# Performance work log

Hardware: AMD Instinct MI355X
Metric: run time of the kernel (lower is better)

The kernel has to match this reference:

```python
import jax, jax.numpy as jnp
import numpy as np

N_NODES, N_EDGES, D_FEAT, HIDDEN, N_CLASSES = 100000, 3200000, 128, 16, 40


def setup_inputs() -> dict:
    key = jax.random.key(0)
    ks = jax.random.split(key, 6)
    x = jax.random.normal(ks[0], (N_NODES, D_FEAT), dtype=jnp.float32)
    edge_index = jax.random.randint(ks[1], (2, N_EDGES), 0, N_NODES, dtype=jnp.int32)
    # SAGEConv params: lin_l (aggregated neighbors, with bias), lin_r (root, no bias)
    W_l = jax.random.normal(ks[2], (D_FEAT, HIDDEN), dtype=jnp.float32) / np.sqrt(D_FEAT)
    b_l = jnp.zeros((HIDDEN,), jnp.float32)
    W_r = jax.random.normal(ks[3], (D_FEAT, HIDDEN), dtype=jnp.float32) / np.sqrt(D_FEAT)
    # final Linear(hidden, num_classes)
    W3 = jax.random.normal(ks[4], (HIDDEN, N_CLASSES), dtype=jnp.float32) / np.sqrt(HIDDEN)
    b3 = jnp.zeros((N_CLASSES,), jnp.float32)
    return {"x": x, "edge_index": edge_index, "W_l": W_l, "b_l": b_l,
            "W_r": W_r, "W3": W3, "b3": b3}


def reference(x, edge_index, W_l, b_l, W_r, W3, b3):
    N = x.shape[0]
    src, dst = edge_index[0], edge_index[1]
    # mean aggregation of source features onto target nodes (PyG source_to_target)
    agg = jax.ops.segment_sum(x[src], dst, num_segments=N)            # [N, F]
    deg = jax.ops.segment_sum(jnp.ones_like(dst, dtype=x.dtype), dst, num_segments=N)
    mean = agg / jnp.maximum(deg, 1.0)[:, None]                        # zero-in-degree -> 0
    # SAGEConv: lin_l(mean) + lin_r(x)
    h = mean @ W_l + b_l + x @ W_r                                     # [N, 16]
    h = jax.nn.relu(h)
    logits = h @ W3 + b3                                               # [N, C]
    return jax.nn.log_softmax(logits, axis=1)
```

## Files before the change

### kernel.cpp

```cpp
#include <hip/hip_runtime.h>
#include <hip/hip_bf16.h>

#define D_FEAT 128
#define HIDDEN 16
#define NCLS 40
#define EPB 4096
#define QSCALE 32.0f
#define QBIAS  8.0f

typedef unsigned int uint;

__global__ __launch_bounds__(256) void p1lin_kernel(
    const int* __restrict__ src, const int* __restrict__ dst,
    int* __restrict__ gcur1, int* __restrict__ buf1,
    int E, int C, int R1, int nb1,
    const float* __restrict__ x,
    const float* __restrict__ Wl, const float* __restrict__ Wr,
    uint* __restrict__ ylb, float* __restrict__ yr, int N) {
  __shared__ __align__(16) char smem[33280];
  int tid = threadIdx.x;

  if (blockIdx.x < nb1) {
    int* lh    = (int*)smem;
    int* loff  = lh + 32;
    int* gbase = loff + 32;
    int* lbuf  = gbase + 32;
    int* ldst  = lbuf + 4096;
    if (tid < 32) lh[tid] = 0;
    __syncthreads();

    int base = blockIdx.x * EPB;
    int key[16], rnk[16], rec[16];
#pragma unroll
    for (int j = 0; j < 16; ++j) {
      int e = base + j * 256 + tid;
      bool ok = e < E;
      int d = ok ? dst[e] : 0;
      int s = ok ? src[e] : 0;
      key[j] = ok ? (d >> 12) : -1;
      rec[j] = s | ((d & 4095) << 17);
      if (ok) rnk[j] = atomicAdd(&lh[key[j]], 1);
    }
    __syncthreads();

    if (tid < 64) {
      int v = (tid < 32) ? lh[tid] : 0;
      int inc = v;
#pragma unroll
      for (int dd = 1; dd < 32; dd <<= 1) {
        int t = __shfl_up(inc, dd);
        if ((int)tid >= dd) inc += t;
      }
      if (tid < 32) {
        loff[tid] = inc - v;
        gbase[tid] = (v && tid < C) ? atomicAdd(&gcur1[tid], v) : 0;
      }
    }
    __syncthreads();

#pragma unroll
    for (int j = 0; j < 16; ++j) {
      if (key[j] >= 0) {
        int p = loff[key[j]] + rnk[j];
        lbuf[p] = rec[j];
        int gp = gbase[key[j]] + rnk[j];
        ldst[p] = (gp < R1) ? key[j] * R1 + gp : -1;
      }
    }
    __syncthreads();

    int tot = min(EPB, E - base);
    for (int i = tid; i < tot; i += 256) {
      int di = ldst[i];
      if (di >= 0) buf1[di] = lbuf[i];
    }
  } else {
    float (*sW)[8][4] = (float(*)[8][4])smem;
    float (*sx)[132]  = (float(*)[132])(smem + 16384);

    for (int idx = tid; idx < D_FEAT * 32; idx += 256) {
      int k = idx >> 5, o = idx & 31;
      float v = (o < 16) ? Wl[k * 16 + o] : Wr[k * 16 + (o - 16)];
      sW[k][o >> 2][o & 3] = v;
    }

    int row0 = (blockIdx.x - nb1) * 32;
    for (int q = tid; q < 32 * 32; q += 256) {
      int r = q >> 5, k4 = q & 31;
      int row = row0 + r;
      float4 v = make_float4(0.f, 0.f, 0.f, 0.f);
      if (row < N) v = *(const float4*)(x + (size_t)row * D_FEAT + k4 * 4);
      *(float4*)(&sx[r][k4 * 4]) = v;
    }
    __syncthreads();

    int r = tid >> 3, oq = tid & 7;
    int row = row0 + r;
    if (row < N) {
      float4 acc = make_float4(0.f, 0.f, 0.f, 0.f);
#pragma unroll
      for (int k = 0; k < D_FEAT; ++k) {
        float xv = sx[r][k];
        const float4 w = *(const float4*)(&sW[k][oq][0]);
        acc.x += xv * w.x; acc.y += xv * w.y;
        acc.z += xv * w.z; acc.w += xv * w.w;
      }
      if (oq < 4) {
        int q0 = __float2int_rn((fminf(fmaxf(acc.x, -7.9f), 7.9f) + QBIAS) * QSCALE);
        int q1 = __float2int_rn((fminf(fmaxf(acc.y, -7.9f), 7.9f) + QBIAS) * QSCALE);
        int q2 = __float2int_rn((fminf(fmaxf(acc.z, -7.9f), 7.9f) + QBIAS) * QSCALE);
        int q3 = __float2int_rn((fminf(fmaxf(acc.w, -7.9f), 7.9f) + QBIAS) * QSCALE);
        uint2 pk;
        pk.x = (uint)q0 | ((uint)q1 << 16);
        pk.y = (uint)q2 | ((uint)q3 << 16);
        *(uint2*)(ylb + (size_t)row * 8 + oq * 2) = pk;
      } else {
        *(float4*)(yr + (size_t)row * 16 + (oq - 4) * 4) = acc;
      }
    }
  }
}

__global__ __launch_bounds__(256) void pass2_kernel(
    const int* __restrict__ buf1, const int* __restrict__ gcur1,
    int* __restrict__ gcur, int* __restrict__ packed,
    int C, int R1, int RF, int chunks) {
  int c = blockIdx.x / chunks;
  int chunk = blockIdx.x - c * chunks;
  int cnt1 = min(gcur1[c], R1);
  int base = chunk * EPB;
  int tot = cnt1 - base;
  if (tot <= 0) return;
  tot = min(tot, EPB);

  __shared__ int lh[32], loff[32], gbase[32];
  __shared__ int lbuf[EPB];
  __shared__ int ldst[EPB];
  int tid = threadIdx.x;
  if (tid < 32) lh[tid] = 0;
  __syncthreads();

  const int* in = buf1 + (size_t)c * R1 + base;
  int key[16], rnk[16], rec[16];
#pragma unroll
  for (int j = 0; j < 16; ++j) {
    int i = j * 256 + tid;
    bool ok = i < tot;
    int r = ok ? in[i] : 0;
    int d12 = (r >> 17) & 4095;
    key[j] = ok ? (d12 >> 7) : -1;
    rec[j] = (r & 0x1FFFF) | ((d12 & 127) << 20);
    if (ok) rnk[j] = atomicAdd(&lh[key[j]], 1);
  }
  __syncthreads();

  if (tid < 64) {
    int v = (tid < 32) ? lh[tid] : 0;
    int inc = v;
#pragma unroll
    for (int dd = 1; dd < 32; dd <<= 1) {
      int t = __shfl_up(inc, dd);
      if ((int)tid >= dd) inc += t;
    }
    if (tid < 32) {
      loff[tid] = inc - v;
      gbase[tid] = v ? atomicAdd(&gcur[c * 32 + tid], v) : 0;
    }
  }
  __syncthreads();

#pragma unroll
  for (int j = 0; j < 16; ++j) {
    if (key[j] >= 0) {
      int p = loff[key[j]] + rnk[j];
      lbuf[p] = rec[j];
      int gp = gbase[key[j]] + rnk[j];
      ldst[p] = (gp < RF) ? (c * 32 + key[j]) * RF + gp : -1;
    }
  }
  __syncthreads();

  for (int i = tid; i < tot; i += 256) {
    int di = ldst[i];
    if (di >= 0) packed[di] = lbuf[i];
  }
}

__global__ __launch_bounds__(1024) void baggrf_kernel(
    const uint* __restrict__ ylb, const int* __restrict__ packed,
    const int* __restrict__ gcur, const float* __restrict__ yr,
    const float* __restrict__ bl, const float* __restrict__ W3,
    const float* __restrict__ b3, float* __restrict__ out,
    int N, int RF) {
  __shared__ uint sagg[128 * 9];
  __shared__ int sdeg[128];
  __shared__ float syr[128 * 16];
  __shared__ float sW3[16 * NCLS];
  __shared__ float sb3[NCLS];
  __shared__ float sbl[16];
  int tid = threadIdx.x;
  int b = blockIdx.x;
  int node0 = b * 128;

  for (int i = tid; i < 128 * 9; i += 1024) sagg[i] = 0u;
  if (tid < 128) sdeg[tid] = 0;
  if (tid >= 384 && tid < 1024) sW3[tid - 384] = W3[tid - 384];
  if (tid < NCLS) sb3[tid] = b3[tid];
  if (tid >= 64 && tid < 80) sbl[tid - 64] = bl[tid - 64];
  __syncthreads();

  int cnt = min(gcur[b], RF);
  int lo = b * RF, hi = lo + cnt;
  for (int e = lo + tid; e < hi; e += 2048) {
    int eb = e + 1024;
    bool has2 = eb < hi;
    int p0 = packed[e];
    int p1 = packed[has2 ? eb : e];
    int s0 = p0 & 0xFFFFF, d0 = (p0 >> 20) & 127;
    int s1 = p1 & 0xFFFFF, d1 = (p1 >> 20) & 127;
    const uint4* q0 = (const uint4*)(ylb + (size_t)s0 * 8);
    const uint4* q1 = (const uint4*)(ylb + (size_t)s1 * 8);
    uint4 a0 = q0[0], a1 = q0[1];
    uint4 b0 = q1[0], b1 = q1[1];

    uint* ip0 = &sagg[d0 * 9];
    atomicAdd(ip0 + 0, a0.x); atomicAdd(ip0 + 1, a0.y);
    atomicAdd(ip0 + 2, a0.z); atomicAdd(ip0 + 3, a0.w);
    atomicAdd(ip0 + 4, a1.x); atomicAdd(ip0 + 5, a1.y);
    atomicAdd(ip0 + 6, a1.z); atomicAdd(ip0 + 7, a1.w);
    atomicAdd(&sdeg[d0], 1);
    if (has2) {
      uint* ip1 = &sagg[d1 * 9];
      atomicAdd(ip1 + 0, b0.x); atomicAdd(ip1 + 1, b0.y);
      atomicAdd(ip1 + 2, b0.z); atomicAdd(ip1 + 3, b0.w);
      atomicAdd(ip1 + 4, b1.x); atomicAdd(ip1 + 5, b1.y);
      atomicAdd(ip1 + 6, b1.z); atomicAdd(ip1 + 7, b1.w);
      atomicAdd(&sdeg[d1], 1);
    }
  }

  int nvalid = min(128, N - node0);
  if (nvalid > 0) {
    int tot16 = nvalid * 16;
    for (int i = tid; i < tot16; i += 1024)
      syr[i] = yr[(size_t)node0 * 16 + i];
  }
  __syncthreads();

  int node = tid >> 3, q = tid & 7;
  int n = node0 + node;
  if (n < N) {
    int dg = sdeg[node];
    float bsub = (QBIAS * QSCALE) * (float)dg;
    float inv = 1.0f / (QSCALE * fmaxf((float)dg, 1.0f));
    float h[16];
#pragma unroll
    for (int j = 0; j < 8; ++j) {
      uint s = sagg[node * 9 + j];
      float v0 = ((float)(s & 0xFFFFu) - bsub) * inv;
      float v1 = ((float)(s >> 16) - bsub) * inv;
      h[2 * j]     = fmaxf(v0 + sbl[2 * j]     + syr[node * 16 + 2 * j], 0.f);
      h[2 * j + 1] = fmaxf(v1 + sbl[2 * j + 1] + syr[node * 16 + 2 * j + 1], 0.f);
    }
    float lg[5];
#pragma unroll
    for (int j = 0; j < 5; ++j) lg[j] = sb3[q * 5 + j];
#pragma unroll
    for (int k = 0; k < 16; ++k) {
      float hv = h[k];
#pragma unroll
      for (int j = 0; j < 5; ++j) lg[j] += hv * sW3[k * NCLS + q * 5 + j];
    }
    float m = lg[0];
#pragma unroll
    for (int j = 1; j < 5; ++j) m = fmaxf(m, lg[j]);
#pragma unroll
    for (int dd = 1; dd < 8; dd <<= 1) m = fmaxf(m, __shfl_xor(m, dd));
    float s = 0.f;
#pragma unroll
    for (int j = 0; j < 5; ++j) s += __expf(lg[j] - m);
#pragma unroll
    for (int dd = 1; dd < 8; dd <<= 1) s += __shfl_xor(s, dd);
    float lse = m + __logf(s);
    float* op = out + (size_t)n * NCLS + q * 5;
#pragma unroll
    for (int j = 0; j < 5; ++j) op[j] = lg[j] - lse;
  }
}

extern "C" void kernel_launch(void* const* d_in, const int* in_sizes, int n_in,
                              void* d_out, int out_size, void* d_ws, size_t ws_size,
                              hipStream_t stream) {
  const float* x   = (const float*)d_in[0];
  const int* eidx  = (const int*)d_in[1];
  const float* Wl  = (const float*)d_in[2];
  const float* bl  = (const float*)d_in[3];
  const float* Wr  = (const float*)d_in[4];
  const float* W3  = (const float*)d_in[5];
  const float* b3  = (const float*)d_in[6];
  float* out = (float*)d_out;

  int N = in_sizes[0] / D_FEAT;
  int E = in_sizes[1] / 2;
  const int* src = eidx;
  const int* dst = eidx + E;

  int C = (N + 4095) >> 12;
  int chunks = (E / C) / EPB + 2;
  int R1 = chunks * EPB;
  int Bf = C * 32;
  int B = (N + 127) >> 7;
  long long m = (long long)E * 128 / N;
  int RF = (int)((m + m / 8 + 511) / 512 * 512);

  size_t n16 = (size_t)N * 16;
  uint* ylb   = (uint*)d_ws;
  float* yr   = (float*)(ylb + (size_t)N * 8);
  int* gcur   = (int*)(yr + n16);
  int* gcur1  = gcur + Bf;
  int* buf1   = gcur1 + C;
  int* packed = buf1 + (size_t)C * R1;

  hipMemsetAsync(gcur, 0, (size_t)(Bf + C) * sizeof(int), stream);

  int nb1 = (E + EPB - 1) / EPB;
  int nblin = (N + 31) / 32;
  p1lin_kernel<<<nb1 + nblin, 256, 0, stream>>>(src, dst, gcur1, buf1,
                                                E, C, R1, nb1,
                                                x, Wl, Wr, ylb, yr, N);

  pass2_kernel<<<C * chunks, 256, 0, stream>>>(buf1, gcur1, gcur, packed,
                                               C, R1, RF, chunks);

  baggrf_kernel<<<B, 1024, 0, stream>>>(ylb, packed, gcur, yr, bl, W3, b3,
                                        out, N, RF);
}
```

Baseline: 95.92 us.

## Move dense linear into pass2 kernel and register-tile rows per thread

Pass 1 now runs as a standalone edge-bucketing kernel, and the dense x@[Wl|Wr] projection is fused into the pass-2 launch instead of pass 1. This balances work between the two launches and shrinks pass-1 shared memory. The linear path now computes 4 rows per thread, reading x straight from global memory rather than staging it in LDS, and pass 2 derives scatter destinations on the fly instead of keeping an ldst array, which halves its LDS use. The trade-off is more registers per thread and uncached global reads of x.

New measurement: 97.83 us. Within noise of the previous version (+2.0%).

```diff
diff --git a/kernel.cpp b/kernel.cpp
--- a/kernel.cpp
+++ b/kernel.cpp
@@ -10,129 +10,14 @@
 
 typedef unsigned int uint;
 
-__global__ __launch_bounds__(256) void p1lin_kernel(
+__device__ __forceinline__ void fma4(float4& a, float s, const float4 w) {
+  a.x += s * w.x; a.y += s * w.y; a.z += s * w.z; a.w += s * w.w;
+}
+
+__global__ __launch_bounds__(256) void pass1_kernel(
     const int* __restrict__ src, const int* __restrict__ dst,
     int* __restrict__ gcur1, int* __restrict__ buf1,
-    int E, int C, int R1, int nb1,
-    const float* __restrict__ x,
-    const float* __restrict__ Wl, const float* __restrict__ Wr,
-    uint* __restrict__ ylb, float* __restrict__ yr, int N) {
-  __shared__ __align__(16) char smem[33280];
-  int tid = threadIdx.x;
-
-  if (blockIdx.x < nb1) {
-    int* lh    = (int*)smem;
-    int* loff  = lh + 32;
-    int* gbase = loff + 32;
-    int* lbuf  = gbase + 32;
-    int* ldst  = lbuf + 4096;
-    if (tid < 32) lh[tid] = 0;
-    __syncthreads();
-
-    int base = blockIdx.x * EPB;
-    int key[16], rnk[16], rec[16];
-#pragma unroll
-    for (int j = 0; j < 16; ++j) {
-      int e = base + j * 256 + tid;
-      bool ok = e < E;
-      int d = ok ? dst[e] : 0;
-      int s = ok ? src[e] : 0;
-      key[j] = ok ? (d >> 12) : -1;
-      rec[j] = s | ((d & 4095) << 17);
-      if (ok) rnk[j] = atomicAdd(&lh[key[j]], 1);
-    }
-    __syncthreads();
-
-    if (tid < 64) {
-      int v = (tid < 32) ? lh[tid] : 0;
-      int inc = v;
-#pragma unroll
-      for (int dd = 1; dd < 32; dd <<= 1) {
-        int t = __shfl_up(inc, dd);
-        if ((int)tid >= dd) inc += t;
-      }
-      if (tid < 32) {
-        loff[tid] = inc - v;
-        gbase[tid] = (v && tid < C) ? atomicAdd(&gcur1[tid], v) : 0;
-      }
-    }
-    __syncthreads();
-
-#pragma unroll
-    for (int j = 0; j < 16; ++j) {
-      if (key[j] >= 0) {
-        int p = loff[key[j]] + rnk[j];
-        lbuf[p] = rec[j];
-        int gp = gbase[key[j]] + rnk[j];
-        ldst[p] = (gp < R1) ? key[j] * R1 + gp : -1;
-      }
-    }
-    __syncthreads();
-
-    int tot = min(EPB, E - base);
-    for (int i = tid; i < tot; i += 256) {
-      int di = ldst[i];
-      if (di >= 0) buf1[di] = lbuf[i];
-    }
-  } else {
-    float (*sW)[8][4] = (float(*)[8][4])smem;
-    float (*sx)[132]  = (float(*)[132])(smem + 16384);
-
-    for (int idx = tid; idx < D_FEAT * 32; idx += 256) {
-      int k = idx >> 5, o = idx & 31;
-      float v = (o < 16) ? Wl[k * 16 + o] : Wr[k * 16 + (o - 16)];
-      sW[k][o >> 2][o & 3] = v;
-    }
-
-    int row0 = (blockIdx.x - nb1) * 32;
-    for (int q = tid; q < 32 * 32; q += 256) {
-      int r = q >> 5, k4 = q & 31;
-      int row = row0 + r;
-      float4 v = make_float4(0.f, 0.f, 0.f, 0.f);
-      if (row < N) v = *(const float4*)(x + (size_t)row * D_FEAT + k4 * 4);
-      *(float4*)(&sx[r][k4 * 4]) = v;
-    }
-    __syncthreads();
-
-    int r = tid >> 3, oq = tid & 7;
-    int row = row0 + r;
-    if (row < N) {
-      float4 acc = make_float4(0.f, 0.f, 0.f, 0.f);
-#pragma unroll
-      for (int k = 0; k < D_FEAT; ++k) {
-        float xv = sx[r][k];
-        const float4 w = *(const float4*)(&sW[k][oq][0]);
-        acc.x += xv * w.x; acc.y += xv * w.y;
-        acc.z += xv * w.z; acc.w += xv * w.w;
-      }
-      if (oq < 4) {
-        int q0 = __float2int_rn((fminf(fmaxf(acc.x, -7.9f), 7.9f) + QBIAS) * QSCALE);
-        int q1 = __float2int_rn((fminf(fmaxf(acc.y, -7.9f), 7.9f) + QBIAS) * QSCALE);
-        int q2 = __float2int_rn((fminf(fmaxf(acc.z, -7.9f), 7.9f) + QBIAS) * QSCALE);
-        int q3 = __float2int_rn((fminf(fmaxf(acc.w, -7.9f), 7.9f) + QBIAS) * QSCALE);
-        uint2 pk;
-        pk.x = (uint)q0 | ((uint)q1 << 16);
-        pk.y = (uint)q2 | ((uint)q3 << 16);
-        *(uint2*)(ylb + (size_t)row * 8 + oq * 2) = pk;
-      } else {
-        *(float4*)(yr + (size_t)row * 16 + (oq - 4) * 4) = acc;
-      }
-    }
-  }
-}
-
-__global__ __launch_bounds__(256) void pass2_kernel(
-    const int* __restrict__ buf1, const int* __restrict__ gcur1,
-    int* __restrict__ gcur, int* __restrict__ packed,
-    int C, int R1, int RF, int chunks) {
-  int c = blockIdx.x / chunks;
-  int chunk = blockIdx.x - c * chunks;
-  int cnt1 = min(gcur1[c], R1);
-  int base = chunk * EPB;
-  int tot = cnt1 - base;
-  if (tot <= 0) return;
-  tot = min(tot, EPB);
-
+    int E, int C, int R1) {
   __shared__ int lh[32], loff[32], gbase[32];
   __shared__ int lbuf[EPB];
   __shared__ int ldst[EPB];
@@ -140,16 +25,16 @@
   if (tid < 32) lh[tid] = 0;
   __syncthreads();
 
-  const int* in = buf1 + (size_t)c * R1 + base;
+  int base = blockIdx.x * EPB;
   int key[16], rnk[16], rec[16];
 #pragma unroll
   for (int j = 0; j < 16; ++j) {
-    int i = j * 256 + tid;
-    bool ok = i < tot;
-    int r = ok ? in[i] : 0;
-    int d12 = (r >> 17) & 4095;
-    key[j] = ok ? (d12 >> 7) : -1;
-    rec[j] = (r & 0x1FFFF) | ((d12 & 127) << 20);
+    int e = base + j * 256 + tid;
+    bool ok = e < E;
+    int d = ok ? dst[e] : 0;
+    int s = ok ? src[e] : 0;
+    key[j] = ok ? (d >> 12) : -1;
+    rec[j] = s | ((d & 4095) << 17);
     if (ok) rnk[j] = atomicAdd(&lh[key[j]], 1);
   }
   __syncthreads();
@@ -164,7 +49,7 @@
     }
     if (tid < 32) {
       loff[tid] = inc - v;
-      gbase[tid] = v ? atomicAdd(&gcur[c * 32 + tid], v) : 0;
+      gbase[tid] = (v && tid < C) ? atomicAdd(&gcur1[tid], v) : 0;
     }
   }
   __syncthreads();
@@ -175,14 +60,152 @@
       int p = loff[key[j]] + rnk[j];
       lbuf[p] = rec[j];
       int gp = gbase[key[j]] + rnk[j];
-      ldst[p] = (gp < RF) ? (c * 32 + key[j]) * RF + gp : -1;
-    }
-  }
-  __syncthreads();
-
+      ldst[p] = (gp < R1) ? key[j] * R1 + gp : -1;
+    }
+  }
+  __syncthreads();
+
+  int tot = min(EPB, E - base);
   for (int i = tid; i < tot; i += 256) {
     int di = ldst[i];
-    if (di >= 0) packed[di] = lbuf[i];
+    if (di >= 0) buf1[di] = lbuf[i];
+  }
+}
+
+__global__ __launch_bounds__(256) void p2lin_kernel(
+    const int* __restrict__ buf1, const int* __restrict__ gcur1,
+    int* __restrict__ gcur, int* __restrict__ packed,
+    int C, int R1, int RF, int chunks, int nb2,
+    const float* __restrict__ x,
+    const float* __restrict__ Wl, const float* __restrict__ Wr,
+    uint* __restrict__ ylb, float* __restrict__ yr, int N) {
+  __shared__ __align__(16) char smem[16896];
+  int tid = threadIdx.x;
+
+  if ((int)blockIdx.x < nb2) {
+    int* lbuf  = (int*)smem;
+    int* lh    = (int*)(smem + 16384);
+    int* loff  = lh + 32;
+    int* gbase = loff + 32;
+
+    int c = blockIdx.x / chunks;
+    int chunk = blockIdx.x - c * chunks;
+    int cnt1 = min(gcur1[c], R1);
+    int base = chunk * EPB;
+    int tot = cnt1 - base;
+    if (tot <= 0) return;
+    tot = min(tot, EPB);
+
+    if (tid < 32) lh[tid] = 0;
+    __syncthreads();
+
+    const int* in = buf1 + (size_t)c * R1 + base;
+    int key[16], rnk[16], rec[16];
+#pragma unroll
+    for (int j = 0; j < 16; ++j) {
+      int i = j * 256 + tid;
+      bool ok = i < tot;
+      int r = ok ? in[i] : 0;
+      key[j] = ok ? ((r >> 24) & 31) : -1;
+      rec[j] = r;
+      if (ok) rnk[j] = atomicAdd(&lh[key[j]], 1);
+    }
+    __syncthreads();
+
+    if (tid < 64) {
+      int v = (tid < 32) ? lh[tid] : 0;
+      int inc = v;
+#pragma unroll
+      for (int dd = 1; dd < 32; dd <<= 1) {
+        int t = __shfl_up(inc, dd);
+        if ((int)tid >= dd) inc += t;
+      }
+      if (tid < 32) {
+        loff[tid] = inc - v;
+        gbase[tid] = v ? atomicAdd(&gcur[c * 32 + tid], v) : 0;
+      }
+    }
+    __syncthreads();
+
+#pragma unroll
+    for (int j = 0; j < 16; ++j)
+      if (key[j] >= 0) lbuf[loff[key[j]] + rnk[j]] = rec[j];
+    __syncthreads();
+
+    for (int i = tid; i < tot; i += 256) {
+      int r = lbuf[i];
+      int k = (r >> 24) & 31;
+      int gp = gbase[k] + (i - loff[k]);
+      if (gp < RF) {
+        int d12 = (r >> 17) & 4095;
+        packed[(size_t)(c * 32 + k) * RF + gp] =
+            (r & 0x1FFFF) | ((d12 & 127) << 20);
+      }
+    }
+  } else {
+    float* sW = (float*)smem;
+    const float4* sWf4 = (const float4*)smem;
+
+    for (int i = tid; i < 4096; i += 256) {
+      int k = i >> 5, c = i & 31;
+      sW[i] = (c < 16) ? Wl[k * 16 + c] : Wr[k * 16 + (c - 16)];
+    }
+    __syncthreads();
+
+    int row0 = ((int)blockIdx.x - nb2) * 128;
+    int quad = tid & 7, rg = tid >> 3;
+    int r0 = row0 + rg * 4;
+    int rr0 = min(r0 + 0, N - 1), rr1 = min(r0 + 1, N - 1);
+    int rr2 = min(r0 + 2, N - 1), rr3 = min(r0 + 3, N - 1);
+    const float* xp0 = x + (size_t)rr0 * D_FEAT;
+    const float* xp1 = x + (size_t)rr1 * D_FEAT;
+    const float* xp2 = x + (size_t)rr2 * D_FEAT;
+    const float* xp3 = x + (size_t)rr3 * D_FEAT;
+
+    float4 acc0 = {0,0,0,0}, acc1 = {0,0,0,0}, acc2 = {0,0,0,0}, acc3 = {0,0,0,0};
+#pragma unroll 4
+    for (int k4 = 0; k4 < 32; ++k4) {
+      float4 x0 = *(const float4*)(xp0 + k4 * 4);
+      float4 x1 = *(const float4*)(xp1 + k4 * 4);
+      float4 x2 = *(const float4*)(xp2 + k4 * 4);
+      float4 x3 = *(const float4*)(xp3 + k4 * 4);
+      float4 w0 = sWf4[(k4 * 4 + 0) * 8 + quad];
+      fma4(acc0, x0.x, w0); fma4(acc1, x1.x, w0);
+      fma4(acc2, x2.x, w0); fma4(acc3, x3.x, w0);
+      float4 w1 = sWf4[(k4 * 4 + 1) * 8 + quad];
+      fma4(acc0, x0.y, w1); fma4(acc1, x1.y, w1);
+      fma4(acc2, x2.y, w1); fma4(acc3, x3.y, w1);
+      float4 w2 = sWf4[(k4 * 4 + 2) * 8 + quad];
+      fma4(acc0, x0.z, w2); fma4(acc1, x1.z, w2);
+      fma4(acc2, x2.z, w2); fma4(acc3, x3.z, w2);
+      float4 w3 = sWf4[(k4 * 4 + 3) * 8 + quad];
+      fma4(acc0, x0.w, w3); fma4(acc1, x1.w, w3);
+      fma4(acc2, x2.w, w3); fma4(acc3, x3.w, w3);
+    }
+
+    float4 accs[4] = {acc0, acc1, acc2, acc3};
+    if (quad < 4) {
+#pragma unroll
+      for (int r = 0; r < 4; ++r) {
+        if (r0 + r < N) {
+          float4 a = accs[r];
+          int q0 = __float2int_rn((fminf(fmaxf(a.x, -7.9f), 7.9f) + QBIAS) * QSCALE);
+          int q1 = __float2int_rn((fminf(fmaxf(a.y, -7.9f), 7.9f) + QBIAS) * QSCALE);
+          int q2 = __float2int_rn((fminf(fmaxf(a.z, -7.9f), 7.9f) + QBIAS) * QSCALE);
+          int q3 = __float2int_rn((fminf(fmaxf(a.w, -7.9f), 7.9f) + QBIAS) * QSCALE);
+          uint2 pk;
+          pk.x = (uint)q0 | ((uint)q1 << 16);
+          pk.y = (uint)q2 | ((uint)q3 << 16);
+          *(uint2*)(ylb + (size_t)(r0 + r) * 8 + quad * 2) = pk;
+        }
+      }
+    } else {
+#pragma unroll
+      for (int r = 0; r < 4; ++r) {
+        if (r0 + r < N)
+          *(float4*)(yr + (size_t)(r0 + r) * 16 + (quad - 4) * 4) = accs[r];
+      }
+    }
   }
 }
 
@@ -324,13 +347,13 @@
   hipMemsetAsync(gcur, 0, (size_t)(Bf + C) * sizeof(int), stream);
 
   int nb1 = (E + EPB - 1) / EPB;
-  int nblin = (N + 31) / 32;
-  p1lin_kernel<<<nb1 + nblin, 256, 0, stream>>>(src, dst, gcur1, buf1,
-                                                E, C, R1, nb1,
+  pass1_kernel<<<nb1, 256, 0, stream>>>(src, dst, gcur1, buf1, E, C, R1);
+
+  int nb2 = C * chunks;
+  int nblin = (N + 127) / 128;
+  p2lin_kernel<<<nb2 + nblin, 256, 0, stream>>>(buf1, gcur1, gcur, packed,
+                                                C, R1, RF, chunks, nb2,
                                                 x, Wl, Wr, ylb, yr, N);
-
-  pass2_kernel<<<C * chunks, 256, 0, stream>>>(buf1, gcur1, gcur, packed,
-                                               C, R1, RF, chunks);
 
   baggrf_kernel<<<B, 1024, 0, stream>>>(ylb, packed, gcur, yr, bl, W3, b3,
                                         out, N, RF);
```
